# Kernel optimization log

Measured on AMD Instinct MI355X. Metric: run time of the kernel, lower is better.

## Reference

```python
import jax, jax.numpy as jnp
import numpy as np

FOOT_Z = (2, 8)
SHANK_Z = (2, 8)
GYRO_LT = jnp.array([3, 4, 5])
GYRO_RT = jnp.array([9, 10, 11])
HF_BIN = 60  # int(30 * TS / SAMPLE_RATE) with TS=256, SAMPLE_RATE=128
EPS = 1e-6


def _std1(x, axis, keepdims=False):
    # torch .std uses unbiased estimator (ddof=1)
    return jnp.std(x, axis=axis, ddof=1, keepdims=keepdims)


def _var1(x, axis):
    return jnp.var(x, axis=axis, ddof=1)


def _kurtosis(x):
    mu = jnp.mean(x, axis=1, keepdims=True)
    std = jnp.clip(_std1(x, 1, keepdims=True), 1e-6, None)
    return jnp.clip(jnp.mean(((x - mu) / std) ** 4, axis=1), -10.0, 30.0)


def _skewness(x):
    mu = jnp.mean(x, axis=1, keepdims=True)
    std = jnp.clip(_std1(x, 1, keepdims=True), 1e-6, None)
    return jnp.clip(jnp.mean(((x - mu) / std) ** 3, axis=1), -10.0, 10.0)


def _zcr(x):
    signs = jnp.sign(x)
    signs = jnp.where(signs == 0, 1.0, signs)
    crosses = (signs[:, 1:] * signs[:, :-1] < 0).astype(jnp.float32)
    return jnp.mean(crosses, axis=1)


def _hf_ratio(x):
    power = jnp.abs(jnp.fft.rfft(x, axis=1)) ** 2  # [B, n_bins]
    total = jnp.sum(power, axis=1) + 1e-6
    hf = jnp.sum(power[:, HF_BIN:], axis=1)
    return hf / total


def _spectral_centroid(x):
    power = jnp.abs(jnp.fft.rfft(x, axis=1)) ** 2  # [B, n_bins]
    n_bins = power.shape[1]
    freqs = jnp.arange(n_bins, dtype=jnp.float32)
    centroid = jnp.sum(freqs * power, axis=1) / (jnp.sum(power, axis=1) + 1e-6)
    return centroid / n_bins


def _impact_duration(x, threshold=0.3):
    pk = jnp.max(jnp.abs(x), axis=1, keepdims=True)
    above = (jnp.abs(x) >= pk * threshold).astype(jnp.float32)
    return jnp.mean(above, axis=1)


def setup_inputs() -> dict:
    key = jax.random.key(0)
    k1, k2, k3 = jax.random.split(key, 3)
    B, C, T = 8192, 12, 256
    foot = jax.random.normal(k1, (B, C, T), jnp.float32)
    shank = jax.random.normal(k2, (B, C, T), jnp.float32)
    thigh = jax.random.normal(k3, (B, C, T), jnp.float32)
    return {"foot": foot, "shank": shank, "thigh": thigh}


def reference(foot, shank, thigh):
    fz_lt = foot[:, FOOT_Z[0], :]
    fz_rt = foot[:, FOOT_Z[1], :]
    sz_lt = shank[:, SHANK_Z[0], :]
    sz_rt = shank[:, SHANK_Z[1], :]

    f_pk_lt = jnp.max(jnp.abs(fz_lt), axis=1)
    f_pk_rt = jnp.max(jnp.abs(fz_rt), axis=1)
    s_pk_lt = jnp.max(jnp.abs(sz_lt), axis=1)
    s_pk_rt = jnp.max(jnp.abs(sz_rt), axis=1)

    ratio_lt = jnp.log1p(f_pk_lt / (s_pk_lt + 1e-4))
    ratio_rt = jnp.log1p(f_pk_rt / (s_pk_rt + 1e-4))

    hf_lt = _hf_ratio(fz_lt)
    hf_rt = _hf_ratio(fz_rt)

    std_lt = _std1(fz_lt, 1)
    std_rt = _std1(fz_rt, 1)

    T_half = fz_lt.shape[1] // 2
    decay_lt = jnp.mean(jnp.abs(fz_lt[:, :T_half]), axis=1) / (jnp.mean(jnp.abs(fz_lt[:, T_half:]), axis=1) + EPS)
    decay_rt = jnp.mean(jnp.abs(fz_rt[:, :T_half]), axis=1) / (jnp.mean(jnp.abs(fz_rt[:, T_half:]), axis=1) + EPS)

    vib_lt = jnp.mean(jnp.abs(sz_lt[:, 1:] - sz_lt[:, :-1]), axis=1)
    vib_rt = jnp.mean(jnp.abs(sz_rt[:, 1:] - sz_rt[:, :-1]), axis=1)

    var_ratio_lt = jnp.log1p(_var1(fz_lt, 1) / (_var1(sz_lt, 1) + 1e-4))
    var_ratio_rt = jnp.log1p(_var1(fz_rt, 1) / (_var1(sz_rt, 1) + 1e-4))

    sc_lt = _spectral_centroid(fz_lt)
    sc_rt = _spectral_centroid(fz_rt)
    dur_lt = _impact_duration(fz_lt)
    dur_rt = _impact_duration(fz_rt)

    fg_lt = foot[:, GYRO_LT, :]
    fg_rt = foot[:, GYRO_RT, :]
    fg_var_lt = jnp.log1p(jnp.sum(_var1(fg_lt, 2), axis=1))
    fg_var_rt = jnp.log1p(jnp.sum(_var1(fg_rt, 2), axis=1))
    fg_peak_lt = jnp.max(jnp.abs(fg_lt), axis=(1, 2))
    fg_peak_rt = jnp.max(jnp.abs(fg_rt), axis=(1, 2))

    sg_lt = shank[:, GYRO_LT, :]
    sg_rt = shank[:, GYRO_RT, :]
    sg_var_lt = jnp.log1p(jnp.sum(_var1(sg_lt, 2), axis=1))
    sg_var_rt = jnp.log1p(jnp.sum(_var1(sg_rt, 2), axis=1))
    sg_peak_lt = jnp.max(jnp.abs(sg_lt), axis=(1, 2))
    sg_peak_rt = jnp.max(jnp.abs(sg_rt), axis=(1, 2))

    tg_lt = thigh[:, GYRO_LT, :]
    tg_rt = thigh[:, GYRO_RT, :]
    tg_var_lt = jnp.log1p(jnp.sum(_var1(tg_lt, 2), axis=1))
    tg_var_rt = jnp.log1p(jnp.sum(_var1(tg_rt, 2), axis=1))
    tg_peak_lt = jnp.max(jnp.abs(tg_lt), axis=(1, 2))
    tg_peak_rt = jnp.max(jnp.abs(tg_rt), axis=(1, 2))

    asym_acc_lt = jnp.abs(f_pk_lt - s_pk_lt)
    asym_acc_rt = jnp.abs(f_pk_rt - s_pk_rt)
    asym_gy_lt = jnp.abs(fg_var_lt - sg_var_lt)
    asym_gy_rt = jnp.abs(fg_var_rt - sg_var_rt)

    foot_rms_lt = jnp.sqrt(jnp.mean(fz_lt ** 2, axis=1))
    foot_rms_rt = jnp.sqrt(jnp.mean(fz_rt ** 2, axis=1))
    shank_rms_lt = jnp.sqrt(jnp.mean(sz_lt ** 2, axis=1))
    shank_rms_rt = jnp.sqrt(jnp.mean(sz_rt ** 2, axis=1))
    trans_lt = jnp.log1p(shank_rms_lt / (foot_rms_lt + EPS))
    trans_rt = jnp.log1p(shank_rms_rt / (foot_rms_rt + EPS))

    kurt_lt = _kurtosis(fz_lt)
    kurt_rt = _kurtosis(fz_rt)
    skew_lt = _skewness(fz_lt)
    skew_rt = _skewness(fz_rt)
    zcr_lt = _zcr(fz_lt)
    zcr_rt = _zcr(fz_rt)

    return jnp.stack([
        f_pk_lt, f_pk_rt, s_pk_lt, s_pk_rt, ratio_lt, ratio_rt, hf_lt, hf_rt,
        std_lt, std_rt, decay_lt, decay_rt, vib_lt, vib_rt,
        var_ratio_lt, var_ratio_rt, sc_lt, sc_rt, dur_lt, dur_rt,
        fg_var_lt, fg_var_rt, fg_peak_lt, fg_peak_rt,
        sg_var_lt, sg_var_rt, sg_peak_lt, sg_peak_rt,
        tg_var_lt, tg_var_rt, tg_peak_lt, tg_peak_rt,
        asym_acc_lt, asym_acc_rt, asym_gy_lt, asym_gy_rt,
        trans_lt, trans_rt, kurt_lt, kurt_rt, skew_lt, skew_rt,
        zcr_lt, zcr_rt,
    ], axis=1)
```

## Files before the change

### kernel.cpp

```cpp
#include <hip/hip_runtime.h>
#include <math.h>


typedef __attribute__((ext_vector_type(8))) short short8;
typedef __attribute__((ext_vector_type(4))) float f32x4;

__device__ __forceinline__ float rdl63(float v){
  return __int_as_float(__builtin_amdgcn_readlane(__float_as_int(v), 63));
}
template<int CTL>
__device__ __forceinline__ float dpp_step_sum(float v){
  return v + __int_as_float(__builtin_amdgcn_update_dpp(0, __float_as_int(v), CTL, 0xF, 0xF, true));
}
template<int CTL>
__device__ __forceinline__ float dpp_step_max(float v){
  return fmaxf(v, __int_as_float(__builtin_amdgcn_update_dpp(0, __float_as_int(v), CTL, 0xF, 0xF, true)));
}
__device__ __forceinline__ float nxt1(float v){
  return __int_as_float(__builtin_amdgcn_update_dpp(0, __float_as_int(v), 0x101, 0xF, 0xF, true));
}
__device__ __forceinline__ float wsum(float v){
  v = dpp_step_sum<0x111>(v); v = dpp_step_sum<0x112>(v); v = dpp_step_sum<0x114>(v);
  v = dpp_step_sum<0x118>(v); v = dpp_step_sum<0x142>(v); v = dpp_step_sum<0x143>(v);
  return rdl63(v);
}
__device__ __forceinline__ float wmax(float v){
  v = dpp_step_max<0x111>(v); v = dpp_step_max<0x112>(v); v = dpp_step_max<0x114>(v);
  v = dpp_step_max<0x118>(v); v = dpp_step_max<0x142>(v); v = dpp_step_max<0x143>(v);
  return rdl63(v);
}
__device__ __forceinline__ float red16hi(float v){
  v = dpp_step_sum<0x111>(v); v = dpp_step_sum<0x112>(v);
  v = dpp_step_sum<0x114>(v); v = dpp_step_sum<0x118>(v);
  return v;
}
__device__ __forceinline__ float sum4(float4 v){ return (v.x+v.y)+(v.z+v.w); }
__device__ __forceinline__ float dot4(float4 v){ return (v.x*v.x+v.y*v.y)+(v.z*v.z+v.w*v.w); }
__device__ __forceinline__ float amax4(float4 v){ return fmaxf(fmaxf(fabsf(v.x),fabsf(v.y)),fmaxf(fabsf(v.z),fabsf(v.w))); }
__device__ __forceinline__ float asum4(float4 v){ return (fabsf(v.x)+fabsf(v.y))+(fabsf(v.z)+fabsf(v.w)); }
__device__ __forceinline__ float clampf(float v,float lo,float hi){ return fminf(fmaxf(v,lo),hi); }
__device__ __forceinline__ unsigned short f2bf(float f){
  unsigned u = __float_as_uint(f);
  return (unsigned short)((u + 0x7FFFu + ((u>>16)&1u)) >> 16);
}

__global__ __launch_bounds__(256) void build_trig(unsigned short* __restrict__ ws){
  int id   = blockIdx.x*256 + threadIdx.x;
  int lane = id & 63;
  int f    = (id>>6) & 1;
  int s    = (id>>7) & 7;
  int T    = (id>>10) & 7;
  int nb   = T*16 + (lane&15);
  int n0   = ((lane>>4)<<3) + (s<<5);
  short8 v;
  #pragma unroll
  for (int j=0;j<8;++j){
    int m = ((n0+j)*nb) & 255;
    if (f) m = (m+192)&255;
    v[j] = (short)f2bf(__cosf((float)m * 0.0245436926066f));
  }
  *(short8*)(ws + (size_t)id*8) = v;
}

__global__ __launch_bounds__(512,4) void biomech_kernel(
    const float* __restrict__ foot, const float* __restrict__ shank,
    const float* __restrict__ thigh, const unsigned short* __restrict__ ws,
    float* __restrict__ out, int B)
{
  const int t    = threadIdx.x;
  const int lane = t & 63;
  const int wv   = t >> 6;

  __shared__ __align__(16) unsigned short sA[16*256];
  __shared__ float sPart[8][16][3];
  __shared__ float sAlt[16];

  const long long b = (long long)blockIdx.x*8 + wv;
  if (b < B) {
    const float* fp = foot  + (size_t)b*3072;
    const float* sp = shank + (size_t)b*3072;
    const float* tp = thigh + (size_t)b*3072;

    float4 xl = ((const float4*)(fp+ 512))[lane];
    float4 xr = ((const float4*)(fp+2048))[lane];
    float4 yl = ((const float4*)(sp+ 512))[lane];
    float4 yr = ((const float4*)(sp+2048))[lane];
    float4 gv[6][3];
    #pragma unroll
    for (int g=0; g<6; ++g){
      const float* bse = (g<2)? fp : (g<4)? sp : tp;
      const float* src = bse + ((g&1)? 2304 : 768);
      gv[g][0] = ((const float4*)src      )[lane];
      gv[g][1] = ((const float4*)(src+256))[lane];
      gv[g][2] = ((const float4*)(src+512))[lane];
    }

    {
      int r0 = 2*wv, r1 = 2*wv+1;
      unsigned lo0 = (unsigned)f2bf(xl.x) | ((unsigned)f2bf(xl.y)<<16);
      unsigned hi0 = (unsigned)f2bf(xl.z) | ((unsigned)f2bf(xl.w)<<16);
      unsigned by0 = (((unsigned)r0<<9) + ((unsigned)lane<<3)) ^ (((unsigned)(r0&7))<<4);
      *(uint2*)((char*)sA + by0) = make_uint2(lo0,hi0);
      unsigned lo1 = (unsigned)f2bf(xr.x) | ((unsigned)f2bf(xr.y)<<16);
      unsigned hi1 = (unsigned)f2bf(xr.z) | ((unsigned)f2bf(xr.w)<<16);
      unsigned by1 = (((unsigned)r1<<9) + ((unsigned)lane<<3)) ^ (((unsigned)(r1&7))<<4);
      *(uint2*)((char*)sA + by1) = make_uint2(lo1,hi1);
    }

    float pk_l  = wmax(amax4(xl)), pk_r  = wmax(amax4(xr));
    float spk_l = wmax(amax4(yl)), spk_r = wmax(amax4(yr));
    float sum_l = wsum(sum4(xl)),  sum_r = wsum(sum4(xr));
    float sq_l  = wsum(dot4(xl)),  sq_r  = wsum(dot4(xr));
    float ssum_l= wsum(sum4(yl)),  ssum_r= wsum(sum4(yr));
    float ssq_l = wsum(dot4(yl)),  ssq_r = wsum(dot4(yr));
    float al = asum4(xl), ar = asum4(xr);
    float h1l = wsum(lane<32 ? al : 0.f), h2l = wsum(lane<32 ? 0.f : al);
    float h1r = wsum(lane<32 ? ar : 0.f), h2r = wsum(lane<32 ? 0.f : ar);
    float alt_l = wsum((xl.x - xl.y) + (xl.z - xl.w));
    float alt_r = wsum((xr.x - xr.y) + (xr.z - xr.w));
    if (lane == 0) { sAlt[2*wv] = alt_l; sAlt[2*wv+1] = alt_r; }

    float mu_l = sum_l*(1.f/256.f), mu_r = sum_r*(1.f/256.f);

    float p3l_c=0.f, p4l_c=0.f, p3r_c=0.f, p4r_c=0.f;
    {
      float p,p2;
      p=xl.x-mu_l; p2=p*p; p3l_c+=p2*p; p4l_c+=p2*p2;
      p=xl.y-mu_l; p2=p*p; p3l_c+=p2*p; p4l_c+=p2*p2;
      p=xl.z-mu_l; p2=p*p; p3l_c+=p2*p; p4l_c+=p2*p2;
      p=xl.w-mu_l; p2=p*p; p3l_c+=p2*p; p4l_c+=p2*p2;
      p=xr.x-mu_r; p2=p*p; p3r_c+=p2*p; p4r_c+=p2*p2;
      p=xr.y-mu_r; p2=p*p; p3r_c+=p2*p; p4r_c+=p2*p2;
      p=xr.z-mu_r; p2=p*p; p3r_c+=p2*p; p4r_c+=p2*p2;
      p=xr.w-mu_r; p2=p*p; p3r_c+=p2*p; p4r_c+=p2*p2;
    }
    float p3l = wsum(p3l_c), p4l = wsum(p4l_c);
    float p3r = wsum(p3r_c), p4r = wsum(p4r_c);

    float thr_l = 0.3f*pk_l, thr_r = 0.3f*pk_r;
    float dl_c = (fabsf(xl.x)>=thr_l?1.f:0.f) + (fabsf(xl.y)>=thr_l?1.f:0.f)
               + (fabsf(xl.z)>=thr_l?1.f:0.f) + (fabsf(xl.w)>=thr_l?1.f:0.f);
    float dr_c = (fabsf(xr.x)>=thr_r?1.f:0.f) + (fabsf(xr.y)>=thr_r?1.f:0.f)
               + (fabsf(xr.z)>=thr_r?1.f:0.f) + (fabsf(xr.w)>=thr_r?1.f:0.f);
    float dur_l = wsum(dl_c), dur_r = wsum(dr_c);

    float nxl = nxt1(xl.x), nxr = nxt1(xr.x);
    float nyl = nxt1(yl.x), nyr = nxt1(yr.x);
    const bool lastl = (lane==63);
    float zl_c = ((xl.x<0.f)!=(xl.y<0.f)?1.f:0.f) + ((xl.y<0.f)!=(xl.z<0.f)?1.f:0.f)
               + ((xl.z<0.f)!=(xl.w<0.f)?1.f:0.f)
               + ((!lastl && ((xl.w<0.f)!=(nxl<0.f)))?1.f:0.f);
    float zr_c = ((xr.x<0.f)!=(xr.y<0.f)?1.f:0.f) + ((xr.y<0.f)!=(xr.z<0.f)?1.f:0.f)
               + ((xr.z<0.f)!=(xr.w<0.f)?1.f:0.f)
               + ((!lastl && ((xr.w<0.f)!=(nxr<0.f)))?1.f:0.f);
    float zc_l = wsum(zl_c), zc_r = wsum(zr_c);
    float vl_c = fabsf(yl.y-yl.x)+fabsf(yl.z-yl.y)+fabsf(yl.w-yl.z) + (lastl?0.f:fabsf(nyl-yl.w));
    float vr_c = fabsf(yr.y-yr.x)+fabsf(yr.z-yr.y)+fabsf(yr.w-yr.z) + (lastl?0.f:fabsf(nyr-yr.w));
    float vib_l = wsum(vl_c), vib_r = wsum(vr_c);

    float gvar[6], gpk[6];
    #pragma unroll
    for (int g=0; g<6; ++g){
      float s0 = wsum(sum4(gv[g][0]));
      float s1 = wsum(sum4(gv[g][1]));
      float s2 = wsum(sum4(gv[g][2]));
      float qt = wsum(dot4(gv[g][0])+dot4(gv[g][1])+dot4(gv[g][2]));
      gpk[g]   = wmax(fmaxf(amax4(gv[g][0]),fmaxf(amax4(gv[g][1]),amax4(gv[g][2]))));
      gvar[g]  = (qt - (s0*s0+s1*s1+s2*s2)*(1.f/256.f))*(1.f/255.f);
    }

    if (lane == 0) {
      float var_fl = fmaxf((sq_l - 256.f*mu_l*mu_l)*(1.f/255.f), 0.f);
      float var_fr = fmaxf((sq_r - 256.f*mu_r*mu_r)*(1.f/255.f), 0.f);
      float std_l = sqrtf(var_fl), std_r = sqrtf(var_fr);
      float inv_l = 1.f/fmaxf(std_l,1e-6f), inv_r = 1.f/fmaxf(std_r,1e-6f);
      float i2l = inv_l*inv_l, i2r = inv_r*inv_r;
      float sk_l = p3l*i2l*inv_l*(1.f/256.f), sk_r = p3r*i2r*inv_r*(1.f/256.f);
      float ku_l = p4l*i2l*i2l*(1.f/256.f),   ku_r = p4r*i2r*i2r*(1.f/256.f);
      float var_sl = fmaxf((ssq_l - ssum_l*ssum_l*(1.f/256.f))*(1.f/255.f), 0.f);
      float var_sr = fmaxf((ssq_r - ssum_r*ssum_r*(1.f/256.f))*(1.f/255.f), 0.f);
      float frms_l = sqrtf(sq_l *(1.f/256.f)), frms_r = sqrtf(sq_r *(1.f/256.f));
      float srms_l = sqrtf(ssq_l*(1.f/256.f)), srms_r = sqrtf(ssq_r*(1.f/256.f));
      float fgv_l = log1pf(gvar[0]), fgv_r = log1pf(gvar[1]);
      float sgv_l = log1pf(gvar[2]), sgv_r = log1pf(gvar[3]);
      float tgv_l = log1pf(gvar[4]), tgv_r = log1pf(gvar[5]);

      float* o = out + (size_t)b*44;
      float4 v0 = {pk_l, pk_r, spk_l, spk_r};
      float2 v4 = {log1pf(pk_l/(spk_l+1e-4f)), log1pf(pk_r/(spk_r+1e-4f))};
      float4 v8 = {std_l, std_r,
                   (h1l*(1.f/128.f))/(h2l*(1.f/128.f)+1e-6f),
                   (h1r*(1.f/128.f))/(h2r*(1.f/128.f)+1e-6f)};
      float4 v12 = {vib_l*(1.f/255.f), vib_r*(1.f/255.f),
                    log1pf(var_fl/(var_sl+1e-4f)), log1pf(var_fr/(var_sr+1e-4f))};
      float2 v18 = {dur_l*(1.f/256.f), dur_r*(1.f/256.f)};
      float4 v20 = {fgv_l, fgv_r, gpk[0], gpk[1]};
      float4 v24 = {sgv_l, sgv_r, gpk[2], gpk[3]};
      float4 v28 = {tgv_l, tgv_r, gpk[4], gpk[5]};
      float4 v32 = {fabsf(pk_l-spk_l), fabsf(pk_r-spk_r),
                    fabsf(fgv_l-sgv_l), fabsf(fgv_r-sgv_r)};
      float4 v36 = {log1pf(srms_l/(frms_l+1e-6f)), log1pf(srms_r/(frms_r+1e-6f)),
                    clampf(ku_l, -10.f, 30.f), clampf(ku_r, -10.f, 30.f)};
      float4 v40 = {clampf(sk_l, -10.f, 10.f), clampf(sk_r, -10.f, 10.f),
                    zc_l*(1.f/255.f), zc_r*(1.f/255.f)};
      *(float4*)(o+0)  = v0;  *(float2*)(o+4)  = v4;
      *(float4*)(o+8)  = v8;  *(float4*)(o+12) = v12;
      *(float2*)(o+18) = v18; *(float4*)(o+20) = v20;
      *(float4*)(o+24) = v24; *(float4*)(o+28) = v28;
      *(float4*)(o+32) = v32; *(float4*)(o+36) = v36;
      *(float4*)(o+40) = v40;
    }
  }

  const int col = lane & 15;
  const int g16 = lane >> 4;
  const int T   = wv;
  const short8* ws8 = (const short8*)ws;
  short8 bc0 = ws8[((T*8+0)*2+0)*64 + lane];
  short8 bs0 = ws8[((T*8+0)*2+1)*64 + lane];
  short8 bc1 = ws8[((T*8+1)*2+0)*64 + lane];
  short8 bs1 = ws8[((T*8+1)*2+1)*64 + lane];
  __syncthreads();

  {
    f32x4 ac={0,0,0,0}, as={0,0,0,0};
    #pragma unroll
    for (int s=0; s<8; ++s){
      unsigned abyte = (((unsigned)col<<9) + ((unsigned)g16<<4) + ((unsigned)s<<6))
                       ^ (((unsigned)(col&7))<<4);
      short8 af = *(const short8*)((const char*)sA + abyte);
      short8 bcn, bsn;
      if (s < 6) {
        bcn = ws8[((T*8+s+2)*2+0)*64 + lane];
        bsn = ws8[((T*8+s+2)*2+1)*64 + lane];
      }
      ac = __builtin_amdgcn_mfma_f32_16x16x32_bf16(af, bc0, ac, 0,0,0);
      as = __builtin_amdgcn_mfma_f32_16x16x32_bf16(af, bs0, as, 0,0,0);
      bc0 = bc1; bs0 = bs1;
      if (s < 6) { bc1 = bcn; bs1 = bsn; }
    }

    float kf = (float)(T*16 + col);
    #pragma unroll
    for (int q=0; q<4; ++q){
      int row = (g16<<2) + q;
      float P = ac[q]*ac[q] + as[q]*as[q];
      float tp = red16hi(P);
      float cp = red16hi(kf*P);
      float hp;
      if (T == 3)      hp = red16hi(col >= 12 ? P : 0.f);
      else if (T >= 4) hp = tp;
      else             hp = 0.f;
      if (col == 15) {
        sPart[T][row][0]=tp; sPart[T][row][1]=hp; sPart[T][row][2]=cp;
      }
    }
  }
  __syncthreads();

  if (t < 16) {
    const int row = t;
    const long long bb = (long long)blockIdx.x*8 + (row>>1);
    if (bb < B) {
      float tot=0.f, hp=0.f, cw=0.f;
      #pragma unroll
      for (int tl=0; tl<8; ++tl){
        tot += sPart[tl][row][0];
        hp  += sPart[tl][row][1];
        cw  += sPart[tl][row][2];
      }
      float a = sAlt[row], P128 = a*a;
      tot += P128; hp += P128; cw = fmaf(128.f, P128, cw);
      int ch = row & 1;
      float* o = out + (size_t)bb*44;
      o[6+ch]  = hp/(tot+1e-6f);
      o[16+ch] = cw/(tot+1e-6f)*(1.f/129.f);
    }
  }
}

extern "C" void kernel_launch(void* const* d_in, const int* in_sizes, int n_in,
                              void* d_out, int out_size, void* d_ws, size_t ws_size,
                              hipStream_t stream) {
  const float* foot  = (const float*)d_in[0];
  const float* shank = (const float*)d_in[1];
  const float* thigh = (const float*)d_in[2];
  float* out = (float*)d_out;
  unsigned short* ws = (unsigned short*)d_ws;
  int B = in_sizes[0] / (12 * 256);
  build_trig<<<dim3(32), dim3(256), 0, stream>>>(ws);
  biomech_kernel<<<dim3((B+7)/8), dim3(512), 0, stream>>>(foot, shank, thigh, ws, out, B);
}
```

Baseline: 52.62 us.

## Split fused kernel into separate stats and DFT kernels

Measured after the change: 68.54 us. 1.3x slower.

```diff
diff --git a/kernel.cpp b/kernel.cpp
--- a/kernel.cpp
+++ b/kernel.cpp
@@ -39,9 +39,9 @@
 __device__ __forceinline__ float amax4(float4 v){ return fmaxf(fmaxf(fabsf(v.x),fabsf(v.y)),fmaxf(fabsf(v.z),fabsf(v.w))); }
 __device__ __forceinline__ float asum4(float4 v){ return (fabsf(v.x)+fabsf(v.y))+(fabsf(v.z)+fabsf(v.w)); }
 __device__ __forceinline__ float clampf(float v,float lo,float hi){ return fminf(fmaxf(v,lo),hi); }
-__device__ __forceinline__ unsigned short f2bf(float f){
+__device__ __forceinline__ unsigned f2bf(float f){
   unsigned u = __float_as_uint(f);
-  return (unsigned short)((u + 0x7FFFu + ((u>>16)&1u)) >> 16);
+  return ((u + 0x7FFFu + ((u>>16)&1u)) >> 16) & 0xFFFFu;
 }
 
 __global__ __launch_bounds__(256) void build_trig(unsigned short* __restrict__ ws){
@@ -62,9 +62,137 @@
   *(short8*)(ws + (size_t)id*8) = v;
 }
 
-__global__ __launch_bounds__(512,4) void biomech_kernel(
+__global__ __launch_bounds__(256,8) void stats_kernel(
     const float* __restrict__ foot, const float* __restrict__ shank,
-    const float* __restrict__ thigh, const unsigned short* __restrict__ ws,
+    const float* __restrict__ thigh, float* __restrict__ out, int B)
+{
+  const int lane = threadIdx.x & 63;
+  const int wv   = threadIdx.x >> 6;
+  const long long b = (long long)blockIdx.x*4 + wv;
+  if (b >= B) return;
+
+  const float* fp = foot  + (size_t)b*3072;
+  const float* sp = shank + (size_t)b*3072;
+  const float* tp = thigh + (size_t)b*3072;
+
+  float4 xl = ((const float4*)(fp+ 512))[lane];
+  float4 xr = ((const float4*)(fp+2048))[lane];
+  float4 yl = ((const float4*)(sp+ 512))[lane];
+  float4 yr = ((const float4*)(sp+2048))[lane];
+  float4 gv[6][3];
+  #pragma unroll
+  for (int g=0; g<6; ++g){
+    const float* bse = (g<2)? fp : (g<4)? sp : tp;
+    const float* src = bse + ((g&1)? 2304 : 768);
+    gv[g][0] = ((const float4*)src      )[lane];
+    gv[g][1] = ((const float4*)(src+256))[lane];
+    gv[g][2] = ((const float4*)(src+512))[lane];
+  }
+
+  float pk_l  = wmax(amax4(xl)), pk_r  = wmax(amax4(xr));
+  float spk_l = wmax(amax4(yl)), spk_r = wmax(amax4(yr));
+  float sum_l = wsum(sum4(xl)),  sum_r = wsum(sum4(xr));
+  float sq_l  = wsum(dot4(xl)),  sq_r  = wsum(dot4(xr));
+  float ssum_l= wsum(sum4(yl)),  ssum_r= wsum(sum4(yr));
+  float ssq_l = wsum(dot4(yl)),  ssq_r = wsum(dot4(yr));
+  float al = asum4(xl), ar = asum4(xr);
+  float h1l = wsum(lane<32 ? al : 0.f), h2l = wsum(lane<32 ? 0.f : al);
+  float h1r = wsum(lane<32 ? ar : 0.f), h2r = wsum(lane<32 ? 0.f : ar);
+
+  float mu_l = sum_l*(1.f/256.f), mu_r = sum_r*(1.f/256.f);
+
+  float p3l_c=0.f, p4l_c=0.f, p3r_c=0.f, p4r_c=0.f;
+  {
+    float p,p2;
+    p=xl.x-mu_l; p2=p*p; p3l_c+=p2*p; p4l_c+=p2*p2;
+    p=xl.y-mu_l; p2=p*p; p3l_c+=p2*p; p4l_c+=p2*p2;
+    p=xl.z-mu_l; p2=p*p; p3l_c+=p2*p; p4l_c+=p2*p2;
+    p=xl.w-mu_l; p2=p*p; p3l_c+=p2*p; p4l_c+=p2*p2;
+    p=xr.x-mu_r; p2=p*p; p3r_c+=p2*p; p4r_c+=p2*p2;
+    p=xr.y-mu_r; p2=p*p; p3r_c+=p2*p; p4r_c+=p2*p2;
+    p=xr.z-mu_r; p2=p*p; p3r_c+=p2*p; p4r_c+=p2*p2;
+    p=xr.w-mu_r; p2=p*p; p3r_c+=p2*p; p4r_c+=p2*p2;
+  }
+  float p3l = wsum(p3l_c), p4l = wsum(p4l_c);
+  float p3r = wsum(p3r_c), p4r = wsum(p4r_c);
+
+  float thr_l = 0.3f*pk_l, thr_r = 0.3f*pk_r;
+  float dl_c = (fabsf(xl.x)>=thr_l?1.f:0.f) + (fabsf(xl.y)>=thr_l?1.f:0.f)
+             + (fabsf(xl.z)>=thr_l?1.f:0.f) + (fabsf(xl.w)>=thr_l?1.f:0.f);
+  float dr_c = (fabsf(xr.x)>=thr_r?1.f:0.f) + (fabsf(xr.y)>=thr_r?1.f:0.f)
+             + (fabsf(xr.z)>=thr_r?1.f:0.f) + (fabsf(xr.w)>=thr_r?1.f:0.f);
+  float dur_l = wsum(dl_c), dur_r = wsum(dr_c);
+
+  float nxl = nxt1(xl.x), nxr = nxt1(xr.x);
+  float nyl = nxt1(yl.x), nyr = nxt1(yr.x);
+  const bool lastl = (lane==63);
+  float zl_c = ((xl.x<0.f)!=(xl.y<0.f)?1.f:0.f) + ((xl.y<0.f)!=(xl.z<0.f)?1.f:0.f)
+             + ((xl.z<0.f)!=(xl.w<0.f)?1.f:0.f)
+             + ((!lastl && ((xl.w<0.f)!=(nxl<0.f)))?1.f:0.f);
+  float zr_c = ((xr.x<0.f)!=(xr.y<0.f)?1.f:0.f) + ((xr.y<0.f)!=(xr.z<0.f)?1.f:0.f)
+             + ((xr.z<0.f)!=(xr.w<0.f)?1.f:0.f)
+             + ((!lastl && ((xr.w<0.f)!=(nxr<0.f)))?1.f:0.f);
+  float zc_l = wsum(zl_c), zc_r = wsum(zr_c);
+  float vl_c = fabsf(yl.y-yl.x)+fabsf(yl.z-yl.y)+fabsf(yl.w-yl.z) + (lastl?0.f:fabsf(nyl-yl.w));
+  float vr_c = fabsf(yr.y-yr.x)+fabsf(yr.z-yr.y)+fabsf(yr.w-yr.z) + (lastl?0.f:fabsf(nyr-yr.w));
+  float vib_l = wsum(vl_c), vib_r = wsum(vr_c);
+
+  float gvar[6], gpk[6];
+  #pragma unroll
+  for (int g=0; g<6; ++g){
+    float s0 = wsum(sum4(gv[g][0]));
+    float s1 = wsum(sum4(gv[g][1]));
+    float s2 = wsum(sum4(gv[g][2]));
+    float qt = wsum(dot4(gv[g][0])+dot4(gv[g][1])+dot4(gv[g][2]));
+    gpk[g]   = wmax(fmaxf(amax4(gv[g][0]),fmaxf(amax4(gv[g][1]),amax4(gv[g][2]))));
+    gvar[g]  = (qt - (s0*s0+s1*s1+s2*s2)*(1.f/256.f))*(1.f/255.f);
+  }
+
+  if (lane == 0) {
+    float var_fl = fmaxf((sq_l - 256.f*mu_l*mu_l)*(1.f/255.f), 0.f);
+    float var_fr = fmaxf((sq_r - 256.f*mu_r*mu_r)*(1.f/255.f), 0.f);
+    float std_l = sqrtf(var_fl), std_r = sqrtf(var_fr);
+    float inv_l = 1.f/fmaxf(std_l,1e-6f), inv_r = 1.f/fmaxf(std_r,1e-6f);
+    float i2l = inv_l*inv_l, i2r = inv_r*inv_r;
+    float sk_l = p3l*i2l*inv_l*(1.f/256.f), sk_r = p3r*i2r*inv_r*(1.f/256.f);
+    float ku_l = p4l*i2l*i2l*(1.f/256.f),   ku_r = p4r*i2r*i2r*(1.f/256.f);
+    float var_sl = fmaxf((ssq_l - ssum_l*ssum_l*(1.f/256.f))*(1.f/255.f), 0.f);
+    float var_sr = fmaxf((ssq_r - ssum_r*ssum_r*(1.f/256.f))*(1.f/255.f), 0.f);
+    float frms_l = sqrtf(sq_l *(1.f/256.f)), frms_r = sqrtf(sq_r *(1.f/256.f));
+    float srms_l = sqrtf(ssq_l*(1.f/256.f)), srms_r = sqrtf(ssq_r*(1.f/256.f));
+    float fgv_l = log1pf(gvar[0]), fgv_r = log1pf(gvar[1]);
+    float sgv_l = log1pf(gvar[2]), sgv_r = log1pf(gvar[3]);
+    float tgv_l = log1pf(gvar[4]), tgv_r = log1pf(gvar[5]);
+
+    float* o = out + (size_t)b*44;
+    float4 v0 = {pk_l, pk_r, spk_l, spk_r};
+    float2 v4 = {log1pf(pk_l/(spk_l+1e-4f)), log1pf(pk_r/(spk_r+1e-4f))};
+    float4 v8 = {std_l, std_r,
+                 (h1l*(1.f/128.f))/(h2l*(1.f/128.f)+1e-6f),
+                 (h1r*(1.f/128.f))/(h2r*(1.f/128.f)+1e-6f)};
+    float4 v12 = {vib_l*(1.f/255.f), vib_r*(1.f/255.f),
+                  log1pf(var_fl/(var_sl+1e-4f)), log1pf(var_fr/(var_sr+1e-4f))};
+    float2 v18 = {dur_l*(1.f/256.f), dur_r*(1.f/256.f)};
+    float4 v20 = {fgv_l, fgv_r, gpk[0], gpk[1]};
+    float4 v24 = {sgv_l, sgv_r, gpk[2], gpk[3]};
+    float4 v28 = {tgv_l, tgv_r, gpk[4], gpk[5]};
+    float4 v32 = {fabsf(pk_l-spk_l), fabsf(pk_r-spk_r),
+                  fabsf(fgv_l-sgv_l), fabsf(fgv_r-sgv_r)};
+    float4 v36 = {log1pf(srms_l/(frms_l+1e-6f)), log1pf(srms_r/(frms_r+1e-6f)),
+                  clampf(ku_l, -10.f, 30.f), clampf(ku_r, -10.f, 30.f)};
+    float4 v40 = {clampf(sk_l, -10.f, 10.f), clampf(sk_r, -10.f, 10.f),
+                  zc_l*(1.f/255.f), zc_r*(1.f/255.f)};
+    *(float4*)(o+0)  = v0;  *(float2*)(o+4)  = v4;
+    *(float4*)(o+8)  = v8;  *(float4*)(o+12) = v12;
+    *(float2*)(o+18) = v18; *(float4*)(o+20) = v20;
+    *(float4*)(o+24) = v24; *(float4*)(o+28) = v28;
+    *(float4*)(o+32) = v32; *(float4*)(o+36) = v36;
+    *(float4*)(o+40) = v40;
+  }
+}
+
+__global__ __launch_bounds__(512,4) void dft_kernel(
+    const float* __restrict__ foot, const unsigned short* __restrict__ ws,
     float* __restrict__ out, int B)
 {
   const int t    = threadIdx.x;
@@ -75,141 +203,21 @@
   __shared__ float sPart[8][16][3];
   __shared__ float sAlt[16];
 
-  const long long b = (long long)blockIdx.x*8 + wv;
-  if (b < B) {
-    const float* fp = foot  + (size_t)b*3072;
-    const float* sp = shank + (size_t)b*3072;
-    const float* tp = thigh + (size_t)b*3072;
-
-    float4 xl = ((const float4*)(fp+ 512))[lane];
-    float4 xr = ((const float4*)(fp+2048))[lane];
-    float4 yl = ((const float4*)(sp+ 512))[lane];
-    float4 yr = ((const float4*)(sp+2048))[lane];
-    float4 gv[6][3];
-    #pragma unroll
-    for (int g=0; g<6; ++g){
-      const float* bse = (g<2)? fp : (g<4)? sp : tp;
-      const float* src = bse + ((g&1)? 2304 : 768);
-      gv[g][0] = ((const float4*)src      )[lane];
-      gv[g][1] = ((const float4*)(src+256))[lane];
-      gv[g][2] = ((const float4*)(src+512))[lane];
+  #pragma unroll
+  for (int p=0; p<2; ++p){
+    int row = p*8 + wv;
+    long long bb = (long long)blockIdx.x*8 + (row>>1);
+    float4 v = {0.f,0.f,0.f,0.f};
+    if (bb < B){
+      const float* src = foot + (size_t)bb*3072 + ((row&1)? 2048 : 512);
+      v = ((const float4*)src)[lane];
     }
-
-    {
-      int r0 = 2*wv, r1 = 2*wv+1;
-      unsigned lo0 = (unsigned)f2bf(xl.x) | ((unsigned)f2bf(xl.y)<<16);
-      unsigned hi0 = (unsigned)f2bf(xl.z) | ((unsigned)f2bf(xl.w)<<16);
-      unsigned by0 = (((unsigned)r0<<9) + ((unsigned)lane<<3)) ^ (((unsigned)(r0&7))<<4);
-      *(uint2*)((char*)sA + by0) = make_uint2(lo0,hi0);
-      unsigned lo1 = (unsigned)f2bf(xr.x) | ((unsigned)f2bf(xr.y)<<16);
-      unsigned hi1 = (unsigned)f2bf(xr.z) | ((unsigned)f2bf(xr.w)<<16);
-      unsigned by1 = (((unsigned)r1<<9) + ((unsigned)lane<<3)) ^ (((unsigned)(r1&7))<<4);
-      *(uint2*)((char*)sA + by1) = make_uint2(lo1,hi1);
-    }
-
-    float pk_l  = wmax(amax4(xl)), pk_r  = wmax(amax4(xr));
-    float spk_l = wmax(amax4(yl)), spk_r = wmax(amax4(yr));
-    float sum_l = wsum(sum4(xl)),  sum_r = wsum(sum4(xr));
-    float sq_l  = wsum(dot4(xl)),  sq_r  = wsum(dot4(xr));
-    float ssum_l= wsum(sum4(yl)),  ssum_r= wsum(sum4(yr));
-    float ssq_l = wsum(dot4(yl)),  ssq_r = wsum(dot4(yr));
-    float al = asum4(xl), ar = asum4(xr);
-    float h1l = wsum(lane<32 ? al : 0.f), h2l = wsum(lane<32 ? 0.f : al);
-    float h1r = wsum(lane<32 ? ar : 0.f), h2r = wsum(lane<32 ? 0.f : ar);
-    float alt_l = wsum((xl.x - xl.y) + (xl.z - xl.w));
-    float alt_r = wsum((xr.x - xr.y) + (xr.z - xr.w));
-    if (lane == 0) { sAlt[2*wv] = alt_l; sAlt[2*wv+1] = alt_r; }
-
-    float mu_l = sum_l*(1.f/256.f), mu_r = sum_r*(1.f/256.f);
-
-    float p3l_c=0.f, p4l_c=0.f, p3r_c=0.f, p4r_c=0.f;
-    {
-      float p,p2;
-      p=xl.x-mu_l; p2=p*p; p3l_c+=p2*p; p4l_c+=p2*p2;
-      p=xl.y-mu_l; p2=p*p; p3l_c+=p2*p; p4l_c+=p2*p2;
-      p=xl.z-mu_l; p2=p*p; p3l_c+=p2*p; p4l_c+=p2*p2;
-      p=xl.w-mu_l; p2=p*p; p3l_c+=p2*p; p4l_c+=p2*p2;
-      p=xr.x-mu_r; p2=p*p; p3r_c+=p2*p; p4r_c+=p2*p2;
-      p=xr.y-mu_r; p2=p*p; p3r_c+=p2*p; p4r_c+=p2*p2;
-      p=xr.z-mu_r; p2=p*p; p3r_c+=p2*p; p4r_c+=p2*p2;
-      p=xr.w-mu_r; p2=p*p; p3r_c+=p2*p; p4r_c+=p2*p2;
-    }
-    float p3l = wsum(p3l_c), p4l = wsum(p4l_c);
-    float p3r = wsum(p3r_c), p4r = wsum(p4r_c);
-
-    float thr_l = 0.3f*pk_l, thr_r = 0.3f*pk_r;
-    float dl_c = (fabsf(xl.x)>=thr_l?1.f:0.f) + (fabsf(xl.y)>=thr_l?1.f:0.f)
-               + (fabsf(xl.z)>=thr_l?1.f:0.f) + (fabsf(xl.w)>=thr_l?1.f:0.f);
-    float dr_c = (fabsf(xr.x)>=thr_r?1.f:0.f) + (fabsf(xr.y)>=thr_r?1.f:0.f)
-               + (fabsf(xr.z)>=thr_r?1.f:0.f) + (fabsf(xr.w)>=thr_r?1.f:0.f);
-    float dur_l = wsum(dl_c), dur_r = wsum(dr_c);
-
-    float nxl = nxt1(xl.x), nxr = nxt1(xr.x);
-    float nyl = nxt1(yl.x), nyr = nxt1(yr.x);
-    const bool lastl = (lane==63);
-    float zl_c = ((xl.x<0.f)!=(xl.y<0.f)?1.f:0.f) + ((xl.y<0.f)!=(xl.z<0.f)?1.f:0.f)
-               + ((xl.z<0.f)!=(xl.w<0.f)?1.f:0.f)
-               + ((!lastl && ((xl.w<0.f)!=(nxl<0.f)))?1.f:0.f);
-    float zr_c = ((xr.x<0.f)!=(xr.y<0.f)?1.f:0.f) + ((xr.y<0.f)!=(xr.z<0.f)?1.f:0.f)
-               + ((xr.z<0.f)!=(xr.w<0.f)?1.f:0.f)
-               + ((!lastl && ((xr.w<0.f)!=(nxr<0.f)))?1.f:0.f);
-    float zc_l = wsum(zl_c), zc_r = wsum(zr_c);
-    float vl_c = fabsf(yl.y-yl.x)+fabsf(yl.z-yl.y)+fabsf(yl.w-yl.z) + (lastl?0.f:fabsf(nyl-yl.w));
-    float vr_c = fabsf(yr.y-yr.x)+fabsf(yr.z-yr.y)+fabsf(yr.w-yr.z) + (lastl?0.f:fabsf(nyr-yr.w));
-    float vib_l = wsum(vl_c), vib_r = wsum(vr_c);
-
-    float gvar[6], gpk[6];
-    #pragma unroll
-    for (int g=0; g<6; ++g){
-      float s0 = wsum(sum4(gv[g][0]));
-      float s1 = wsum(sum4(gv[g][1]));
-      float s2 = wsum(sum4(gv[g][2]));
-      float qt = wsum(dot4(gv[g][0])+dot4(gv[g][1])+dot4(gv[g][2]));
-      gpk[g]   = wmax(fmaxf(amax4(gv[g][0]),fmaxf(amax4(gv[g][1]),amax4(gv[g][2]))));
-      gvar[g]  = (qt - (s0*s0+s1*s1+s2*s2)*(1.f/256.f))*(1.f/255.f);
-    }
-
-    if (lane == 0) {
-      float var_fl = fmaxf((sq_l - 256.f*mu_l*mu_l)*(1.f/255.f), 0.f);
-      float var_fr = fmaxf((sq_r - 256.f*mu_r*mu_r)*(1.f/255.f), 0.f);
-      float std_l = sqrtf(var_fl), std_r = sqrtf(var_fr);
-      float inv_l = 1.f/fmaxf(std_l,1e-6f), inv_r = 1.f/fmaxf(std_r,1e-6f);
-      float i2l = inv_l*inv_l, i2r = inv_r*inv_r;
-      float sk_l = p3l*i2l*inv_l*(1.f/256.f), sk_r = p3r*i2r*inv_r*(1.f/256.f);
-      float ku_l = p4l*i2l*i2l*(1.f/256.f),   ku_r = p4r*i2r*i2r*(1.f/256.f);
-      float var_sl = fmaxf((ssq_l - ssum_l*ssum_l*(1.f/256.f))*(1.f/255.f), 0.f);
-      float var_sr = fmaxf((ssq_r - ssum_r*ssum_r*(1.f/256.f))*(1.f/255.f), 0.f);
-      float frms_l = sqrtf(sq_l *(1.f/256.f)), frms_r = sqrtf(sq_r *(1.f/256.f));
-      float srms_l = sqrtf(ssq_l*(1.f/256.f)), srms_r = sqrtf(ssq_r*(1.f/256.f));
-      float fgv_l = log1pf(gvar[0]), fgv_r = log1pf(gvar[1]);
-      float sgv_l = log1pf(gvar[2]), sgv_r = log1pf(gvar[3]);
-      float tgv_l = log1pf(gvar[4]), tgv_r = log1pf(gvar[5]);
-
-      float* o = out + (size_t)b*44;
-      float4 v0 = {pk_l, pk_r, spk_l, spk_r};
-      float2 v4 = {log1pf(pk_l/(spk_l+1e-4f)), log1pf(pk_r/(spk_r+1e-4f))};
-      float4 v8 = {std_l, std_r,
-                   (h1l*(1.f/128.f))/(h2l*(1.f/128.f)+1e-6f),
-                   (h1r*(1.f/128.f))/(h2r*(1.f/128.f)+1e-6f)};
-      float4 v12 = {vib_l*(1.f/255.f), vib_r*(1.f/255.f),
-                    log1pf(var_fl/(var_sl+1e-4f)), log1pf(var_fr/(var_sr+1e-4f))};
-      float2 v18 = {dur_l*(1.f/256.f), dur_r*(1.f/256.f)};
-      float4 v20 = {fgv_l, fgv_r, gpk[0], gpk[1]};
-      float4 v24 = {sgv_l, sgv_r, gpk[2], gpk[3]};
-      float4 v28 = {tgv_l, tgv_r, gpk[4], gpk[5]};
-      float4 v32 = {fabsf(pk_l-spk_l), fabsf(pk_r-spk_r),
-                    fabsf(fgv_l-sgv_l), fabsf(fgv_r-sgv_r)};
-      float4 v36 = {log1pf(srms_l/(frms_l+1e-6f)), log1pf(srms_r/(frms_r+1e-6f)),
-                    clampf(ku_l, -10.f, 30.f), clampf(ku_r, -10.f, 30.f)};
-      float4 v40 = {clampf(sk_l, -10.f, 10.f), clampf(sk_r, -10.f, 10.f),
-                    zc_l*(1.f/255.f), zc_r*(1.f/255.f)};
-      *(float4*)(o+0)  = v0;  *(float2*)(o+4)  = v4;
-      *(float4*)(o+8)  = v8;  *(float4*)(o+12) = v12;
-      *(float2*)(o+18) = v18; *(float4*)(o+20) = v20;
-      *(float4*)(o+24) = v24; *(float4*)(o+28) = v28;
-      *(float4*)(o+32) = v32; *(float4*)(o+36) = v36;
-      *(float4*)(o+40) = v40;
-    }
+    float alt = wsum((v.x - v.y) + (v.z - v.w));
+    if (lane == 0) sAlt[row] = alt;
+    unsigned lo = f2bf(v.x) | (f2bf(v.y)<<16);
+    unsigned hi = f2bf(v.z) | (f2bf(v.w)<<16);
+    unsigned by = (((unsigned)row<<9) + ((unsigned)lane<<3)) ^ (((unsigned)(row&7))<<4);
+    *(uint2*)((char*)sA + by) = make_uint2(lo,hi);
   }
 
   const int col = lane & 15;
@@ -289,5 +297,6 @@
   unsigned short* ws = (unsigned short*)d_ws;
   int B = in_sizes[0] / (12 * 256);
   build_trig<<<dim3(32), dim3(256), 0, stream>>>(ws);
-  biomech_kernel<<<dim3((B+7)/8), dim3(512), 0, stream>>>(foot, shank, thigh, ws, out, B);
-}
+  stats_kernel<<<dim3((B+3)/4), dim3(256), 0, stream>>>(foot, shank, thigh, out, B);
+  dft_kernel<<<dim3((B+7)/8), dim3(512), 0, stream>>>(foot, ws, out, B);
+}
```
